# Kernel optimization log

Hardware: AMD Instinct MI355X
Metric: run time of the kernel (lower is better)

The kernel has to match this reference:

```python
import jax, jax.numpy as jnp
import numpy as np


def setup_inputs() -> dict:
    key = jax.random.key(0)
    k1, k2, k3, k4 = jax.random.split(key, 4)
    N, T, F = 8192, 128, 9
    M_s = 256
    merged = jax.random.normal(k1, (N, T, F), dtype=jnp.float32)
    input1 = jax.random.normal(k2, (N, T, F), dtype=jnp.float32)
    samples = jax.random.normal(k3, (N, M_s), dtype=jnp.float32)
    labels = jax.random.randint(k4, (N,), 0, 10, dtype=jnp.int32)
    return {"merged": merged, "input1": input1, "samples": samples, "labels": labels}


def reference(merged, input1, samples, labels):
    # Pairwise squared distances S_ij = sum_k (s_i - s_j)^2 / M_s, computed via
    # the Gram-matrix identity instead of materializing the [N, N, M_s] tensor.
    M_s = samples.shape[1]
    sq = jnp.sum(samples * samples, axis=-1)                 # [N]
    gram = jnp.einsum('im,jm->ij', samples, samples)         # [N, N]
    S_ij = (sq[:, None] + sq[None, :] - 2.0 * gram) / jnp.float32(M_s)
    same = (labels[:, None] == labels[None, :]).astype(jnp.float32)
    term2 = jnp.mean(jnp.maximum(0.0, (1.0 - same) * (1.0 - S_ij)))
    L_label = 10.0 * jnp.mean(same * S_ij) + 10.0 * term2
    return L_label
```

## Files before the change

### kernel.cpp

```cpp
#include <hip/hip_runtime.h>
#include <hip/hip_bf16.h>

#define NROWS 8192
#define KDIM  256
#define NT    64
#define NBLK  (NT * (NT + 1) / 2)
#define GRID  512

typedef __attribute__((ext_vector_type(4))) float f32x4;

#define GLD(gp, lp)                                                            \
  __builtin_amdgcn_global_load_lds(                                            \
      (const __attribute__((address_space(1))) void*)(gp),                     \
      (__attribute__((address_space(3))) void*)(lp), 16, 0, 0)

__global__ void prep_kernel(const float* __restrict__ samples,
                            unsigned char* __restrict__ sf8,
                            float* __restrict__ sq,
                            float* __restrict__ accg) {
  int t = threadIdx.x, lane = t & 63, wv = t >> 6;
  int row = blockIdx.x * 4 + wv;
  float4 v = ((const float4*)samples)[(size_t)row * 64 + lane];
  int pk0 = __builtin_amdgcn_cvt_pk_fp8_f32(v.x, v.y, 0, false);
  int pk1 = __builtin_amdgcn_cvt_pk_fp8_f32(v.z, v.w, 0, false);
  ((unsigned int*)sf8)[(size_t)row * 64 + lane] =
      (unsigned)(pk0 & 0xffff) | ((unsigned)pk1 << 16);
  float p = v.x * v.x + v.y * v.y + v.z * v.z + v.w * v.w;
#pragma unroll
  for (int off = 32; off; off >>= 1) p += __shfl_down(p, off);
  if (lane == 0) sq[row] = p;
  if (row == 0 && lane < 2) accg[lane] = 0.0f;
}

__device__ inline void decode_tile(int b, int& bi, int& bj) {
  float disc = (2.0f * NT + 1.0f) * (2.0f * NT + 1.0f) - 8.0f * (float)b;
  bi = (int)(((2.0f * NT + 1.0f) - sqrtf(disc)) * 0.5f);
  if (bi < 0) bi = 0;
  if (bi > NT - 1) bi = NT - 1;
  while (bi > 0 && (bi * NT - bi * (bi - 1) / 2) > b) --bi;
  while (((bi + 1) * NT - (bi + 1) * bi / 2) <= b) ++bi;
  bj = bi + (b - (bi * NT - bi * (bi - 1) / 2));
}

#define LOAD_A(BI)                                                             \
  {                                                                            \
    _Pragma("unroll") for (int i = 0; i < 2; i++) {                            \
      const unsigned char* Ar =                                                \
          sf8 + (size_t)((BI) * 128 + wm * 32 + i * 16 + r) * KDIM + ko * 8;   \
      _Pragma("unroll") for (int kc = 0; kc < 8; kc++)                         \
          af[i][kc] = *(const long*)(Ar + kc * 32);                            \
    }                                                                          \
    _Pragma("unroll") for (int i = 0; i < 2; i++)                              \
        _Pragma("unroll") for (int q = 0; q < 4; q++) {                        \
      int gr = (BI) * 128 + wm * 32 + i * 16 + q4 + q;                         \
      sqa[i * 4 + q] = sq[gr];                                                 \
      laa[i * 4 + q] = labels[gr];                                             \
    }                                                                          \
  }

#define STAGE_B(BJ, BUF)                                                       \
  {                                                                            \
    _Pragma("unroll") for (int p = 0; p < 4; ++p) {                            \
      int region = p * 8 + w;                                                  \
      int rr = region * 4 + lr;                                                \
      int c = pc ^ (rr & 15);                                                  \
      GLD(sf8 + (size_t)((BJ) * 128 + rr) * KDIM + c * 16,                     \
          &Bs[BUF][region * 1024]);                                            \
    }                                                                          \
  }

__global__ __launch_bounds__(512) void pair_kernel(
    const unsigned char* __restrict__ sf8, const float* __restrict__ sq,
    const int* __restrict__ labels, float* __restrict__ accg) {

  __shared__ __align__(16) unsigned char Bs[2][32 * 1024];

  int t = threadIdx.x;
  int lane = t & 63;
  int w = t >> 6;
  int wm = w >> 1, wn = w & 1;
  int lr = lane >> 4, pc = lane & 15;
  int r = lane & 15;
  int ko = lane >> 4;
  int kq = ko >> 1, hf = (ko & 1) * 8;
  int q4 = ko * 4;

  int t0 = (blockIdx.x * 65) >> 4;
  int t1 = ((blockIdx.x + 1) * 65) >> 4;
  int bi, bj;
  decode_tile(t0, bi, bj);

  long af[2][8];
  float sqa[8];
  int laa[8];

  int abi = bi;
  LOAD_A(bi);
  STAGE_B(bj, 0);
  int cur = 0;
  float s1t = 0.f, s2t = 0.f;

  for (int tile = t0; tile < t1; ++tile) {
    __syncthreads();

    float sqb[4];
    int lab[4];
#pragma unroll
    for (int j = 0; j < 4; j++) {
      int gc = bj * 128 + wn * 64 + j * 16 + r;
      sqb[j] = sq[gc];
      lab[j] = labels[gc];
    }

    if (bi != abi) { LOAD_A(bi); abi = bi; }

    int nbi = bi, nbj = bj + 1;
    if (nbj == NT) { ++nbi; nbj = nbi; }
    if (tile + 1 < t1) STAGE_B(nbj, cur ^ 1);

    f32x4 acc[2][4];
#pragma unroll
    for (int i = 0; i < 2; i++)
#pragma unroll
      for (int j = 0; j < 4; j++) acc[i][j] = (f32x4){0.f, 0.f, 0.f, 0.f};

#pragma unroll
    for (int kc = 0; kc < 8; ++kc) {
      long bfr[4];
#pragma unroll
      for (int j = 0; j < 4; j++) {
        int n = wn * 64 + j * 16 + r;
        bfr[j] =
            *(const long*)(&Bs[cur][n * 256 + (((kc * 2 + kq) ^ r) * 16) + hf]);
      }
#pragma unroll
      for (int i = 0; i < 2; i++)
#pragma unroll
        for (int j = 0; j < 4; j++)
          acc[i][j] = __builtin_amdgcn_mfma_f32_16x16x32_fp8_fp8(
              af[i][kc], bfr[j], acc[i][j], 0, 0, 0);
    }

    float s1 = 0.f, s2 = 0.f;
#pragma unroll
    for (int j = 0; j < 4; j++) {
#pragma unroll
      for (int i = 0; i < 2; i++) {
#pragma unroll
        for (int q = 0; q < 4; q++) {
          float S = (sqa[i * 4 + q] + sqb[j] - 2.0f * acc[i][j][q]) *
                    (1.0f / 256.0f);
          if (laa[i * 4 + q] == lab[j]) s1 += S;
          else                          s2 += fmaxf(0.f, 1.f - S);
        }
      }
    }
    float wt = (bi == bj) ? 1.0f : 2.0f;
    s1t += wt * s1;
    s2t += wt * s2;

    bi = nbi; bj = nbj; cur ^= 1;
  }

#pragma unroll
  for (int off = 32; off; off >>= 1) {
    s1t += __shfl_down(s1t, off);
    s2t += __shfl_down(s2t, off);
  }
  __syncthreads();
  float* red = (float*)&Bs[0][0];
  if (lane == 0) { red[w] = s1t; red[8 + w] = s2t; }
  __syncthreads();
  if (t == 0) {
    float a = 0.f, b2 = 0.f;
#pragma unroll
    for (int k = 0; k < 8; k++) { a += red[k]; b2 += red[8 + k]; }
    atomicAdd(&accg[0], a);
    atomicAdd(&accg[1], b2);
  }
}

__global__ void finalize_kernel(const float* __restrict__ accg,
                                float* __restrict__ out) {
  out[0] = 10.0f * (accg[0] + accg[1]) *
           (1.0f / ((float)NROWS * (float)NROWS));
}

extern "C" void kernel_launch(void* const* d_in, const int* in_sizes, int n_in,
                              void* d_out, int out_size, void* d_ws,
                              size_t ws_size, hipStream_t stream) {
  const float* samples = (const float*)d_in[2];
  const int*   labels  = (const int*)d_in[3];

  char* ws = (char*)d_ws;
  unsigned char* sf8 = (unsigned char*)ws;
  float* sq   = (float*)(ws + (size_t)NROWS * KDIM);
  float* accg = (float*)(ws + (size_t)NROWS * KDIM + NROWS * 4);
  float* out  = (float*)d_out;

  prep_kernel<<<NROWS / 4, 256, 0, stream>>>(samples, sf8, sq, accg);
  pair_kernel<<<GRID, 512, 0, stream>>>(sf8, sq, labels, accg);
  finalize_kernel<<<1, 1, 0, stream>>>(accg, out);
}
```

Before: 143.7 us.

## Give each wave a private B-strip in LDS and drop per-tile block barriers

Each wave now stages its own 32-column strip of the B tile into a private LDS region and computes a 64x32 sub-tile (4x2 MFMA blocks), so the per-iteration __syncthreads is replaced by explicit vmcnt waits. Grid is halved to 256 blocks, each doing roughly twice as many tiles, and LDS grows to 128KB per block. This removes block-wide barrier stalls but increases LDS footprint and A-register usage, and the hand-written vmcnt waits depend on the compiler's load ordering.

```diff
diff --git a/kernel.cpp b/kernel.cpp
--- a/kernel.cpp
+++ b/kernel.cpp
@@ -5,7 +5,7 @@
 #define KDIM  256
 #define NT    64
 #define NBLK  (NT * (NT + 1) / 2)
-#define GRID  512
+#define GRID  256
 
 typedef __attribute__((ext_vector_type(4))) float f32x4;
 
@@ -44,15 +44,16 @@
 
 #define LOAD_A(BI)                                                             \
   {                                                                            \
-    _Pragma("unroll") for (int i = 0; i < 2; i++) {                            \
+    _Pragma("unroll") for (int i = 0; i < 4; i++) {                            \
       const unsigned char* Ar =                                                \
-          sf8 + (size_t)((BI) * 128 + wm * 32 + i * 16 + r) * KDIM + ko * 8;   \
+          sf8 +                                                                \
+          (size_t)((BI) * 128 + rowhalf * 64 + i * 16 + r) * KDIM + ko * 8;    \
       _Pragma("unroll") for (int kc = 0; kc < 8; kc++)                         \
           af[i][kc] = *(const long*)(Ar + kc * 32);                            \
     }                                                                          \
-    _Pragma("unroll") for (int i = 0; i < 2; i++)                              \
+    _Pragma("unroll") for (int i = 0; i < 4; i++)                              \
         _Pragma("unroll") for (int q = 0; q < 4; q++) {                        \
-      int gr = (BI) * 128 + wm * 32 + i * 16 + q4 + q;                         \
+      int gr = (BI) * 128 + rowhalf * 64 + i * 16 + q4 + q;                    \
       sqa[i * 4 + q] = sq[gr];                                                 \
       laa[i * 4 + q] = labels[gr];                                             \
     }                                                                          \
@@ -60,12 +61,11 @@
 
 #define STAGE_B(BJ, BUF)                                                       \
   {                                                                            \
-    _Pragma("unroll") for (int p = 0; p < 4; ++p) {                            \
-      int region = p * 8 + w;                                                  \
-      int rr = region * 4 + lr;                                                \
-      int c = pc ^ (rr & 15);                                                  \
-      GLD(sf8 + (size_t)((BJ) * 128 + rr) * KDIM + c * 16,                     \
-          &Bs[BUF][region * 1024]);                                            \
+    _Pragma("unroll") for (int p = 0; p < 8; ++p) {                            \
+      int rel = p * 4 + lr4;                                                   \
+      int c = pc ^ (rel & 15);                                                 \
+      GLD(sf8 + (size_t)((BJ) * 128 + colstrip * 32 + rel) * KDIM + c * 16,    \
+          &Bs[wbase + (BUF) * 8192 + p * 1024]);                               \
     }                                                                          \
   }
 
@@ -73,26 +73,27 @@
     const unsigned char* __restrict__ sf8, const float* __restrict__ sq,
     const int* __restrict__ labels, float* __restrict__ accg) {
 
-  __shared__ __align__(16) unsigned char Bs[2][32 * 1024];
+  __shared__ __align__(16) unsigned char Bs[131072];
 
   int t = threadIdx.x;
   int lane = t & 63;
   int w = t >> 6;
-  int wm = w >> 1, wn = w & 1;
-  int lr = lane >> 4, pc = lane & 15;
+  int rowhalf = w & 1, colstrip = w >> 1;
+  int wbase = w * 16384;
+  int lr4 = lane >> 4, pc = lane & 15;
   int r = lane & 15;
   int ko = lane >> 4;
   int kq = ko >> 1, hf = (ko & 1) * 8;
   int q4 = ko * 4;
 
-  int t0 = (blockIdx.x * 65) >> 4;
-  int t1 = ((blockIdx.x + 1) * 65) >> 4;
+  int t0 = (blockIdx.x * 65) >> 3;
+  int t1 = ((blockIdx.x + 1) * 65) >> 3;
   int bi, bj;
   decode_tile(t0, bi, bj);
 
-  long af[2][8];
-  float sqa[8];
-  int laa[8];
+  long af[4][8];
+  float sqa[16];
+  int laa[16];
 
   int abi = bi;
   LOAD_A(bi);
@@ -101,13 +102,11 @@
   float s1t = 0.f, s2t = 0.f;
 
   for (int tile = t0; tile < t1; ++tile) {
-    __syncthreads();
-
-    float sqb[4];
-    int lab[4];
-#pragma unroll
-    for (int j = 0; j < 4; j++) {
-      int gc = bj * 128 + wn * 64 + j * 16 + r;
+    float sqb[2];
+    int lab[2];
+#pragma unroll
+    for (int j = 0; j < 2; j++) {
+      int gc = bj * 128 + colstrip * 32 + j * 16 + r;
       sqb[j] = sq[gc];
       lab[j] = labels[gc];
     }
@@ -116,36 +115,40 @@
 
     int nbi = bi, nbj = bj + 1;
     if (nbj == NT) { ++nbi; nbj = nbi; }
-    if (tile + 1 < t1) STAGE_B(nbj, cur ^ 1);
-
-    f32x4 acc[2][4];
-#pragma unroll
-    for (int i = 0; i < 2; i++)
-#pragma unroll
-      for (int j = 0; j < 4; j++) acc[i][j] = (f32x4){0.f, 0.f, 0.f, 0.f};
+    if (tile + 1 < t1) {
+      STAGE_B(nbj, cur ^ 1);
+      asm volatile("s_waitcnt vmcnt(8)" ::: "memory");
+    } else {
+      asm volatile("s_waitcnt vmcnt(0)" ::: "memory");
+    }
+
+    f32x4 acc[4][2];
+#pragma unroll
+    for (int i = 0; i < 4; i++)
+#pragma unroll
+      for (int j = 0; j < 2; j++) acc[i][j] = (f32x4){0.f, 0.f, 0.f, 0.f};
 
 #pragma unroll
     for (int kc = 0; kc < 8; ++kc) {
-      long bfr[4];
-#pragma unroll
-      for (int j = 0; j < 4; j++) {
-        int n = wn * 64 + j * 16 + r;
-        bfr[j] =
-            *(const long*)(&Bs[cur][n * 256 + (((kc * 2 + kq) ^ r) * 16) + hf]);
+      long bfr[2];
+#pragma unroll
+      for (int j = 0; j < 2; j++) {
+        bfr[j] = *(const long*)(&Bs[wbase + cur * 8192 + (j * 16 + r) * 256 +
+                                    (((kc * 2 + kq) ^ r) * 16) + hf]);
       }
 #pragma unroll
-      for (int i = 0; i < 2; i++)
-#pragma unroll
-        for (int j = 0; j < 4; j++)
+      for (int i = 0; i < 4; i++)
+#pragma unroll
+        for (int j = 0; j < 2; j++)
           acc[i][j] = __builtin_amdgcn_mfma_f32_16x16x32_fp8_fp8(
               af[i][kc], bfr[j], acc[i][j], 0, 0, 0);
     }
 
     float s1 = 0.f, s2 = 0.f;
 #pragma unroll
-    for (int j = 0; j < 4; j++) {
-#pragma unroll
-      for (int i = 0; i < 2; i++) {
+    for (int j = 0; j < 2; j++) {
+#pragma unroll
+      for (int i = 0; i < 4; i++) {
 #pragma unroll
         for (int q = 0; q < 4; q++) {
           float S = (sqa[i * 4 + q] + sqb[j] - 2.0f * acc[i][j][q]) *
@@ -168,7 +171,7 @@
     s2t += __shfl_down(s2t, off);
   }
   __syncthreads();
-  float* red = (float*)&Bs[0][0];
+  float* red = (float*)&Bs[0];
   if (lane == 0) { red[w] = s1t; red[8 + w] = s2t; }
   __syncthreads();
   if (t == 0) {
```

Measured after the change: 148.1 us. 3.1% more time.
